# Kernel tuning notes

Measured on AMD Instinct MI355X. Metric: run time of the kernel, lower is better.

The kernel has to match this reference:

```python
import jax, jax.numpy as jnp
import numpy as np

N, DN, DE, L, FE = 1024, 128, 128, 4, 5

def setup_inputs() -> dict:
    key = jax.random.key(0)
    ks = jax.random.split(key, 20)
    f = lambda k, shape, fan: jax.random.normal(k, shape, dtype=jnp.float32) / np.sqrt(fan)
    h = jax.random.normal(ks[0], (1, N, DN), dtype=jnp.float32)
    e = jax.random.normal(ks[1], (1, N, N, DE), dtype=jnp.float32)
    adj = (jax.random.uniform(ks[2], (1, N, N)) < 0.03).astype(jnp.float32)  # sparse-ish dense adjacency
    edge = jax.random.normal(ks[3], (FE,), dtype=jnp.float32)
    return {
        'h': h, 'e': e, 'adj': adj, 'edge': edge,
        # message linear over concat(h_j, e_ij), split into node/edge parts
        'w_msg_h': f(ks[4], (DN, DN), DN + DE),
        'w_msg_e': f(ks[5], (DN, DE), DN + DE),
        'b_msg':   jnp.zeros((DN,), jnp.float32),
        # GRUCell params (torch layout: gates r,z,n stacked)
        'w_ih': f(ks[6], (3 * DN, DN), DN),
        'w_hh': f(ks[7], (3 * DN, DN), DN),
        'b_ih': jnp.zeros((3 * DN,), jnp.float32),
        'b_hh': jnp.zeros((3 * DN,), jnp.float32),
        # gated-sum readout to graph vector of size DE
        'w_gate': f(ks[8], (DE, 2 * DN), 2 * DN),
        'b_gate': jnp.zeros((DE,), jnp.float32),
        'w_out':  f(ks[9], (DE, 2 * DN), 2 * DN),
        'b_out':  jnp.zeros((DE,), jnp.float32),
        # edge embedding (no bias) and final fc
        'w_embed': f(ks[10], (DE, FE), FE),
        'w_fc':    f(ks[11], (DE, 2 * DE), 2 * DE),
        'b_fc':    jnp.zeros((DE,), jnp.float32),
    }


def reference(h, e, adj, edge, w_msg_h, w_msg_e, b_msg, w_ih, w_hh, b_ih, b_hh,
              w_gate, b_gate, w_out, b_out, w_embed, w_fc, b_fc):
    h0 = h
    # edge part of the message is layer-independent: precompute once [1,N,N,DN]
    e_msg = jnp.einsum('bijf,df->bijd', e, w_msg_e)
    for _ in range(L):
        # m_i = sum_j adj_ij * (W_h h_j + W_e e_ij) + b
        m = (jnp.einsum('bij,bjd->bid', adj, h @ w_msg_h.T)
             + jnp.einsum('bij,bijd->bid', adj, e_msg) + b_msg)
        gi = m @ w_ih.T + b_ih
        gh = h @ w_hh.T + b_hh
        gir, giz, gin = jnp.split(gi, 3, axis=-1)
        ghr, ghz, ghn = jnp.split(gh, 3, axis=-1)
        r = jax.nn.sigmoid(gir + ghr)
        z = jax.nn.sigmoid(giz + ghz)
        n = jnp.tanh(gin + r * ghn)
        h = (1.0 - z) * n + z * h
    # gated-sum readout over nodes -> graph vector [1, DE]
    hc = jnp.concatenate([h, h0], axis=-1)
    gv = jnp.sum(jax.nn.sigmoid(hc @ w_gate.T + b_gate) * jnp.tanh(hc @ w_out.T + b_out), axis=1)
    gv = gv.squeeze(0)                      # [DE]
    ee = w_embed @ edge                     # [DE]
    init_edge = jnp.concatenate([gv, ee], axis=-1) @ w_fc.T + b_fc  # [DE]
    return init_edge
```

## Files before the change

kernel.cpp:

```cpp
#include <hip/hip_runtime.h>

__device__ __forceinline__ float sigm(float x){ return 1.f / (1.f + __expf(-x)); }

constexpr int N = 1024, D = 128, CAP = 192;

constexpr int OFF_WT_ME   = 0;
constexpr int OFF_WT_MH   = OFF_WT_ME   + 128*128;
constexpr int OFF_WT_IH   = OFF_WT_MH   + 128*128;
constexpr int OFF_WT_HH   = OFF_WT_IH   + 128*384;
constexpr int OFF_WT_GATE = OFF_WT_HH   + 128*384;
constexpr int OFF_WT_OUT  = OFF_WT_GATE + 256*128;
constexpr int OFF_WT_FC   = OFF_WT_OUT  + 256*128;
constexpr int OFF_EE      = OFF_WT_FC   + 256*128;
constexpr int OFF_GV      = OFF_EE + 128;
constexpr int OFF_EC      = OFF_GV + 128;
constexpr int OFF_HCUR    = OFF_EC   + N*D;
constexpr int OFF_HW      = OFF_HCUR + N*D;
constexpr int OFF_CNT     = OFF_HW   + N*D;
constexpr int OFF_NZI     = OFF_CNT  + N;
constexpr int OFF_NZV     = OFF_NZI  + N*CAP;

constexpr int PT0 = OFF_WT_MH, PT1 = OFF_WT_IH, PT2 = OFF_WT_HH, PT3 = OFF_WT_GATE,
              PT4 = OFF_WT_OUT, PT5 = OFF_WT_FC, PT6 = OFF_EE, PT7 = OFF_GV,
              PT8 = OFF_EC;

__global__ __launch_bounds__(256)
void k_prep(const float* w_me, const float* w_mh, const float* w_ih, const float* w_hh,
            const float* w_gate, const float* w_out, const float* w_fc,
            const float* w_embed, const float* edge, float* ws){
  int idx = blockIdx.x * 256 + threadIdx.x;
  if (idx < PT0)      { int k = idx;       int f = k >> 7, d = k & 127; ws[idx] = w_me[d*128 + f]; }
  else if (idx < PT1) { int k = idx - PT0; int f = k >> 7, d = k & 127; ws[idx] = w_mh[d*128 + f]; }
  else if (idx < PT2) { int k = idx - PT1; int f = k / 384, o = k % 384; ws[idx] = w_ih[o*128 + f]; }
  else if (idx < PT3) { int k = idx - PT2; int f = k / 384, o = k % 384; ws[idx] = w_hh[o*128 + f]; }
  else if (idx < PT4) { int k = idx - PT3; int f = k >> 7, c = k & 127; ws[idx] = w_gate[c*256 + f]; }
  else if (idx < PT5) { int k = idx - PT4; int f = k >> 7, c = k & 127; ws[idx] = w_out[c*256 + f]; }
  else if (idx < PT6) { int k = idx - PT5; int c = k >> 7, o = k & 127; ws[idx] = w_fc[o*256 + c]; }
  else if (idx < PT7) { int c = idx - PT6; float a = 0.f;
                        for (int q = 0; q < 5; ++q) a += w_embed[c*5 + q] * edge[q];
                        ws[idx] = a; }
  else if (idx < PT8) { ws[idx] = 0.f; }
}

__global__ __launch_bounds__(256)
void k_gather(const float* adj, const float* e, const float* h, const float* b_msg, float* ws){
  __shared__ int   cnt_sh;
  __shared__ int   idx_sh[CAP];
  __shared__ float val_sh[CAP];
  __shared__ float red_sh[512];
  __shared__ float ea_sh[128];
  const int i = blockIdx.x, t = threadIdx.x;
  if (t == 0) cnt_sh = 0;
  __syncthreads();
  const float* arow = adj + (size_t)i * N;
  #pragma unroll
  for (int q = 0; q < 4; ++q){
    int j = t + q*256;
    float v = arow[j];
    if (v != 0.f){
      int p = atomicAdd(&cnt_sh, 1);
      if (p < CAP){ idx_sh[p] = j; val_sh[p] = v; }
    }
  }
  __syncthreads();
  const int cnt = min(cnt_sh, CAP);
  int*   cntp = (int*)(ws + OFF_CNT);
  int*   nzi  = (int*)(ws + OFF_NZI);
  float* nzv  = ws + OFF_NZV;
  if (t == 0) cntp[i] = cnt;
  for (int k = t; k < cnt; k += 256){ nzi[(size_t)i*CAP + k] = idx_sh[k]; nzv[(size_t)i*CAP + k] = val_sh[k]; }

  const int lane = t & 63, wv = t >> 6;
  float ax = 0.f, ay = 0.f;
  const float* eb = e + ((size_t)i << 17);
  for (int k = wv; k < cnt; k += 4){
    int j = idx_sh[k]; float v = val_sh[k];
    float2 uu = *(const float2*)(eb + (size_t)j*128 + 2*lane);
    ax += v * uu.x;
    ay += v * uu.y;
  }
  red_sh[wv*128 + 2*lane]     = ax;
  red_sh[wv*128 + 2*lane + 1] = ay;
  __syncthreads();
  if (t < 128) ea_sh[t] = red_sh[t] + red_sh[128+t] + red_sh[256+t] + red_sh[384+t];
  __syncthreads();

  const float* wT = ws + OFF_WT_ME;
  const int d = t & 127, half = t >> 7;
  float acc = 0.f;
  for (int f = half*64; f < half*64 + 64; ++f) acc += ea_sh[f] * wT[f*128 + d];
  red_sh[half*128 + d] = acc;
  __syncthreads();
  if (t < 128){
    ws[OFF_EC   + (size_t)i*128 + t] = red_sh[t] + red_sh[128 + t] + b_msg[t];
    ws[OFF_HCUR + (size_t)i*128 + t] = h[(size_t)i*128 + t];
  }
}

__global__ __launch_bounds__(128)
void k_hw(float* ws){
  __shared__ float h_sh[8][128];
  const int t = threadIdx.x, i0 = blockIdx.x * 8;
  const float* hc = ws + OFF_HCUR;
  #pragma unroll
  for (int n = 0; n < 8; ++n) h_sh[n][t] = hc[(size_t)(i0+n)*128 + t];
  __syncthreads();
  const float* wT = ws + OFF_WT_MH;
  float acc[8] = {};
  for (int f = 0; f < 128; ++f){
    float w = wT[f*128 + t];
    #pragma unroll
    for (int n = 0; n < 8; ++n) acc[n] += w * h_sh[n][f];
  }
  float* hw = ws + OFF_HW;
  #pragma unroll
  for (int n = 0; n < 8; ++n) hw[(size_t)(i0+n)*128 + t] = acc[n];
}

__global__ __launch_bounds__(384)
void k_gru(const float* b_ih, const float* b_hh, float* ws){
  __shared__ float m_sh[4][128], h_sh[4][128];
  __shared__ float sr_sh[4][128], sz_sh[4][128], gn_sh[4][128], hn_sh[4][128];
  const int t = threadIdx.x, i0 = blockIdx.x * 4;
  float* hc = ws + OFF_HCUR;
  const float* hw = ws + OFF_HW;
  const float* ec = ws + OFF_EC;
  const int*   cntp = (const int*)(ws + OFF_CNT);
  const int*   nzi  = (const int*)(ws + OFF_NZI);
  const float* nzv  = ws + OFF_NZV;
  for (int idx = t; idx < 512; idx += 384){
    int n = idx >> 7, c = idx & 127, i = i0 + n;
    h_sh[n][c] = hc[(size_t)i*128 + c];
    float a = ec[(size_t)i*128 + c];
    const int cn = cntp[i];
    const int*   ji = nzi + (size_t)i*CAP;
    const float* jv = nzv + (size_t)i*CAP;
    for (int k = 0; k < cn; ++k) a += jv[k] * hw[(size_t)ji[k]*128 + c];
    m_sh[n][c] = a;
  }
  __syncthreads();
  const float* wi_ = ws + OFF_WT_IH;
  const float* wh_ = ws + OFF_WT_HH;
  float ag[4] = {}, ah[4] = {};
  for (int f = 0; f < 128; ++f){
    float wi = wi_[f*384 + t], wh = wh_[f*384 + t];
    #pragma unroll
    for (int n = 0; n < 4; ++n){ ag[n] += wi * m_sh[n][f]; ah[n] += wh * h_sh[n][f]; }
  }
  const float bi = b_ih[t], bh = b_hh[t];
  if (t < 128){
    #pragma unroll
    for (int n = 0; n < 4; ++n) sr_sh[n][t] = ag[n] + ah[n] + bi + bh;
  } else if (t < 256){
    const int c = t - 128;
    #pragma unroll
    for (int n = 0; n < 4; ++n) sz_sh[n][c] = ag[n] + ah[n] + bi + bh;
  } else {
    const int c = t - 256;
    #pragma unroll
    for (int n = 0; n < 4; ++n){ gn_sh[n][c] = ag[n] + bi; hn_sh[n][c] = ah[n] + bh; }
  }
  __syncthreads();
  for (int idx = t; idx < 512; idx += 384){
    int n = idx >> 7, c = idx & 127;
    float r  = sigm(sr_sh[n][c]);
    float z  = sigm(sz_sh[n][c]);
    float nn = tanhf(gn_sh[n][c] + r * hn_sh[n][c]);
    hc[(size_t)(i0+n)*128 + c] = (1.f - z) * nn + z * h_sh[n][c];
  }
}

__global__ __launch_bounds__(128)
void k_readout(const float* h0, const float* b_gate, const float* b_out, float* ws){
  __shared__ float hc_sh[8][256];
  const int t = threadIdx.x, i0 = blockIdx.x * 8;
  const float* hcur = ws + OFF_HCUR;
  #pragma unroll
  for (int n = 0; n < 8; ++n){
    hc_sh[n][t]       = hcur[(size_t)(i0+n)*128 + t];
    hc_sh[n][128 + t] = h0[(size_t)(i0+n)*128 + t];
  }
  __syncthreads();
  const float* wg_ = ws + OFF_WT_GATE;
  const float* wo_ = ws + OFF_WT_OUT;
  float ag[8] = {}, ao[8] = {};
  for (int f = 0; f < 256; ++f){
    float wg = wg_[f*128 + t], wo = wo_[f*128 + t];
    #pragma unroll
    for (int n = 0; n < 8; ++n){ ag[n] += wg * hc_sh[n][f]; ao[n] += wo * hc_sh[n][f]; }
  }
  const float bg = b_gate[t], bo = b_out[t];
  float s = 0.f;
  #pragma unroll
  for (int n = 0; n < 8; ++n) s += sigm(ag[n] + bg) * tanhf(ao[n] + bo);
  atomicAdd(ws + OFF_GV + t, s);
}

__global__ __launch_bounds__(128)
void k_fc(const float* b_fc, float* out, const float* ws){
  const int o = threadIdx.x;
  const float* wT = ws + OFF_WT_FC;
  const float* gv = ws + OFF_GV;
  const float* ee = ws + OFF_EE;
  float acc = b_fc[o];
  for (int c = 0; c < 128; ++c) acc += gv[c] * wT[c*128 + o];
  for (int c = 0; c < 128; ++c) acc += ee[c] * wT[(128 + c)*128 + o];
  out[o] = acc;
}

extern "C" void kernel_launch(void* const* d_in, const int* in_sizes, int n_in,
                              void* d_out, int out_size, void* d_ws, size_t ws_size,
                              hipStream_t stream){
  const float* h      = (const float*)d_in[0];
  const float* e      = (const float*)d_in[1];
  const float* adj    = (const float*)d_in[2];
  const float* edge   = (const float*)d_in[3];
  const float* w_mh   = (const float*)d_in[4];
  const float* w_me   = (const float*)d_in[5];
  const float* b_msg  = (const float*)d_in[6];
  const float* w_ih   = (const float*)d_in[7];
  const float* w_hh   = (const float*)d_in[8];
  const float* b_ih   = (const float*)d_in[9];
  const float* b_hh   = (const float*)d_in[10];
  const float* w_gate = (const float*)d_in[11];
  const float* b_gate = (const float*)d_in[12];
  const float* w_out  = (const float*)d_in[13];
  const float* b_out  = (const float*)d_in[14];
  const float* w_emb  = (const float*)d_in[15];
  const float* w_fc   = (const float*)d_in[16];
  const float* b_fc   = (const float*)d_in[17];
  float* ws = (float*)d_ws;

  k_prep<<<(PT8 + 255) / 256, 256, 0, stream>>>(w_me, w_mh, w_ih, w_hh, w_gate,
                                                w_out, w_fc, w_emb, edge, ws);
  k_gather<<<N, 256, 0, stream>>>(adj, e, h, b_msg, ws);
  for (int l = 0; l < 4; ++l){
    k_hw <<<N/8, 128, 0, stream>>>(ws);
    k_gru<<<N/4, 384, 0, stream>>>(b_ih, b_hh, ws);
  }
  k_readout<<<N/8, 128, 0, stream>>>(h, b_gate, b_out, ws);
  k_fc<<<1, 128, 0, stream>>>(b_fc, (float*)d_out, ws);
}
```

Before: 804.1 us.

## Fold message weight into GRU input weight and hoist constant edge term

New measurement: 789.0 us. Within noise of the previous version (-1.9%).

```diff
diff --git a/kernel.cpp b/kernel.cpp
--- a/kernel.cpp
+++ b/kernel.cpp
@@ -1,45 +1,56 @@
 #include <hip/hip_runtime.h>
 
+
 __device__ __forceinline__ float sigm(float x){ return 1.f / (1.f + __expf(-x)); }
 
 constexpr int N = 1024, D = 128, CAP = 192;
 
 constexpr int OFF_WT_ME   = 0;
-constexpr int OFF_WT_MH   = OFF_WT_ME   + 128*128;
-constexpr int OFF_WT_IH   = OFF_WT_MH   + 128*128;
+constexpr int OFF_WT_IH   = OFF_WT_ME   + 128*128;
 constexpr int OFF_WT_HH   = OFF_WT_IH   + 128*384;
 constexpr int OFF_WT_GATE = OFF_WT_HH   + 128*384;
 constexpr int OFF_WT_OUT  = OFF_WT_GATE + 256*128;
 constexpr int OFF_WT_FC   = OFF_WT_OUT  + 256*128;
 constexpr int OFF_EE      = OFF_WT_FC   + 256*128;
 constexpr int OFF_GV      = OFF_EE + 128;
-constexpr int OFF_EC      = OFF_GV + 128;
-constexpr int OFF_HCUR    = OFF_EC   + N*D;
-constexpr int OFF_HW      = OFF_HCUR + N*D;
-constexpr int OFF_CNT     = OFF_HW   + N*D;
-constexpr int OFF_NZI     = OFF_CNT  + N;
-constexpr int OFF_NZV     = OFF_NZI  + N*CAP;
-
-constexpr int PT0 = OFF_WT_MH, PT1 = OFF_WT_IH, PT2 = OFF_WT_HH, PT3 = OFF_WT_GATE,
-              PT4 = OFF_WT_OUT, PT5 = OFF_WT_FC, PT6 = OFF_EE, PT7 = OFF_GV,
-              PT8 = OFF_EC;
+constexpr int OFF_WCT     = OFF_GV + 128;
+constexpr int OFF_C       = OFF_WCT + 128*384;
+constexpr int OFF_EC      = OFF_C   + N*384;
+constexpr int OFF_HA      = OFF_EC  + N*D;
+constexpr int OFF_HB      = OFF_HA  + N*D;
+constexpr int OFF_CNT     = OFF_HB  + N*D;
+constexpr int OFF_NZI     = OFF_CNT + N;
+constexpr int OFF_NZV     = OFF_NZI + N*CAP;
+
+constexpr int PT0 = OFF_WT_IH, PT1 = OFF_WT_HH, PT2 = OFF_WT_GATE, PT3 = OFF_WT_OUT,
+              PT4 = OFF_WT_FC, PT5 = OFF_EE, PT6 = OFF_GV, PT7 = OFF_WCT;
 
 __global__ __launch_bounds__(256)
-void k_prep(const float* w_me, const float* w_mh, const float* w_ih, const float* w_hh,
+void k_prep(const float* w_me, const float* w_ih, const float* w_hh,
             const float* w_gate, const float* w_out, const float* w_fc,
             const float* w_embed, const float* edge, float* ws){
   int idx = blockIdx.x * 256 + threadIdx.x;
   if (idx < PT0)      { int k = idx;       int f = k >> 7, d = k & 127; ws[idx] = w_me[d*128 + f]; }
-  else if (idx < PT1) { int k = idx - PT0; int f = k >> 7, d = k & 127; ws[idx] = w_mh[d*128 + f]; }
-  else if (idx < PT2) { int k = idx - PT1; int f = k / 384, o = k % 384; ws[idx] = w_ih[o*128 + f]; }
-  else if (idx < PT3) { int k = idx - PT2; int f = k / 384, o = k % 384; ws[idx] = w_hh[o*128 + f]; }
-  else if (idx < PT4) { int k = idx - PT3; int f = k >> 7, c = k & 127; ws[idx] = w_gate[c*256 + f]; }
-  else if (idx < PT5) { int k = idx - PT4; int f = k >> 7, c = k & 127; ws[idx] = w_out[c*256 + f]; }
-  else if (idx < PT6) { int k = idx - PT5; int c = k >> 7, o = k & 127; ws[idx] = w_fc[o*256 + c]; }
-  else if (idx < PT7) { int c = idx - PT6; float a = 0.f;
+  else if (idx < PT1) { int k = idx - PT0; int f = k / 384, o = k % 384; ws[idx] = w_ih[o*128 + f]; }
+  else if (idx < PT2) { int k = idx - PT1; int f = k / 384, o = k % 384; ws[idx] = w_hh[o*128 + f]; }
+  else if (idx < PT3) { int k = idx - PT2; int f = k >> 7, c = k & 127; ws[idx] = w_gate[c*256 + f]; }
+  else if (idx < PT4) { int k = idx - PT3; int f = k >> 7, c = k & 127; ws[idx] = w_out[c*256 + f]; }
+  else if (idx < PT5) { int k = idx - PT4; int c = k >> 7, o = k & 127; ws[idx] = w_fc[o*256 + c]; }
+  else if (idx < PT6) { int c = idx - PT5; float a = 0.f;
                         for (int q = 0; q < 5; ++q) a += w_embed[c*5 + q] * edge[q];
                         ws[idx] = a; }
-  else if (idx < PT8) { ws[idx] = 0.f; }
+  else if (idx < PT7) { ws[idx] = 0.f; }
+}
+
+__global__ __launch_bounds__(128)
+void k_wc(const float* w_ih, const float* w_mh, float* ws){
+  __shared__ float ih_sh[128];
+  const int o = blockIdx.x, t = threadIdx.x;
+  ih_sh[t] = w_ih[o*128 + t];
+  __syncthreads();
+  float acc = 0.f;
+  for (int d = 0; d < 128; ++d) acc += ih_sh[d] * w_mh[d*128 + t];
+  ws[OFF_WCT + t*384 + o] = acc;
 }
 
 __global__ __launch_bounds__(256)
@@ -92,73 +103,77 @@
   red_sh[half*128 + d] = acc;
   __syncthreads();
   if (t < 128){
-    ws[OFF_EC   + (size_t)i*128 + t] = red_sh[t] + red_sh[128 + t] + b_msg[t];
-    ws[OFF_HCUR + (size_t)i*128 + t] = h[(size_t)i*128 + t];
-  }
-}
-
-__global__ __launch_bounds__(128)
-void k_hw(float* ws){
-  __shared__ float h_sh[8][128];
-  const int t = threadIdx.x, i0 = blockIdx.x * 8;
-  const float* hc = ws + OFF_HCUR;
-  #pragma unroll
-  for (int n = 0; n < 8; ++n) h_sh[n][t] = hc[(size_t)(i0+n)*128 + t];
-  __syncthreads();
-  const float* wT = ws + OFF_WT_MH;
-  float acc[8] = {};
+    ws[OFF_EC + (size_t)i*128 + t] = red_sh[t] + red_sh[128 + t] + b_msg[t];
+    ws[OFF_HA + (size_t)i*128 + t] = h[(size_t)i*128 + t];
+  }
+}
+
+__global__ __launch_bounds__(384)
+void k_cprep(const float* b_ih, float* ws){
+  __shared__ float ec_sh[4][128];
+  const int t = threadIdx.x, i0 = blockIdx.x * 4;
+  const float* ec = ws + OFF_EC;
+  for (int idx = t; idx < 512; idx += 384){
+    int n = idx >> 7, c = idx & 127;
+    ec_sh[n][c] = ec[(size_t)(i0+n)*128 + c];
+  }
+  __syncthreads();
+  const float* wi_ = ws + OFF_WT_IH;
+  float acc[4] = {};
   for (int f = 0; f < 128; ++f){
-    float w = wT[f*128 + t];
-    #pragma unroll
-    for (int n = 0; n < 8; ++n) acc[n] += w * h_sh[n][f];
-  }
-  float* hw = ws + OFF_HW;
-  #pragma unroll
-  for (int n = 0; n < 8; ++n) hw[(size_t)(i0+n)*128 + t] = acc[n];
+    float w = wi_[f*384 + t];
+    #pragma unroll
+    for (int n = 0; n < 4; ++n) acc[n] += w * ec_sh[n][f];
+  }
+  const float bi = b_ih[t];
+  float* C = ws + OFF_C;
+  #pragma unroll
+  for (int n = 0; n < 4; ++n) C[(size_t)(i0+n)*384 + t] = acc[n] + bi;
 }
 
 __global__ __launch_bounds__(384)
-void k_gru(const float* b_ih, const float* b_hh, float* ws){
-  __shared__ float m_sh[4][128], h_sh[4][128];
+void k_layer(const float* b_hh, const float* hA, float* hB, float* ws){
+  __shared__ float hs_sh[4][128], h_sh[4][128];
   __shared__ float sr_sh[4][128], sz_sh[4][128], gn_sh[4][128], hn_sh[4][128];
   const int t = threadIdx.x, i0 = blockIdx.x * 4;
-  float* hc = ws + OFF_HCUR;
-  const float* hw = ws + OFF_HW;
-  const float* ec = ws + OFF_EC;
   const int*   cntp = (const int*)(ws + OFF_CNT);
   const int*   nzi  = (const int*)(ws + OFF_NZI);
   const float* nzv  = ws + OFF_NZV;
   for (int idx = t; idx < 512; idx += 384){
     int n = idx >> 7, c = idx & 127, i = i0 + n;
-    h_sh[n][c] = hc[(size_t)i*128 + c];
-    float a = ec[(size_t)i*128 + c];
+    h_sh[n][c] = hA[(size_t)i*128 + c];
+    float a = 0.f;
     const int cn = cntp[i];
     const int*   ji = nzi + (size_t)i*CAP;
     const float* jv = nzv + (size_t)i*CAP;
-    for (int k = 0; k < cn; ++k) a += jv[k] * hw[(size_t)ji[k]*128 + c];
-    m_sh[n][c] = a;
-  }
-  __syncthreads();
-  const float* wi_ = ws + OFF_WT_IH;
+    for (int k = 0; k < cn; ++k) a += jv[k] * hA[(size_t)ji[k]*128 + c];
+    hs_sh[n][c] = a;
+  }
+  __syncthreads();
+  const float* wc_ = ws + OFF_WCT;
   const float* wh_ = ws + OFF_WT_HH;
   float ag[4] = {}, ah[4] = {};
   for (int f = 0; f < 128; ++f){
-    float wi = wi_[f*384 + t], wh = wh_[f*384 + t];
-    #pragma unroll
-    for (int n = 0; n < 4; ++n){ ag[n] += wi * m_sh[n][f]; ah[n] += wh * h_sh[n][f]; }
-  }
-  const float bi = b_ih[t], bh = b_hh[t];
+    float wi = wc_[f*384 + t], wh = wh_[f*384 + t];
+    #pragma unroll
+    for (int n = 0; n < 4; ++n){ ag[n] += wi * hs_sh[n][f]; ah[n] += wh * h_sh[n][f]; }
+  }
+  const float* C = ws + OFF_C;
+  float cv[4];
+  #pragma unroll
+  for (int n = 0; n < 4; ++n) cv[n] = C[(size_t)(i0+n)*384 + t];
+  const float bh = b_hh[t];
   if (t < 128){
     #pragma unroll
-    for (int n = 0; n < 4; ++n) sr_sh[n][t] = ag[n] + ah[n] + bi + bh;
+    for (int n = 0; n < 4; ++n) sr_sh[n][t] = ag[n] + cv[n] + ah[n] + bh;
   } else if (t < 256){
     const int c = t - 128;
     #pragma unroll
-    for (int n = 0; n < 4; ++n) sz_sh[n][c] = ag[n] + ah[n] + bi + bh;
+    for (int n = 0; n < 4; ++n) sz_sh[n][c] = ag[n] + cv[n] + ah[n] + bh;
   } else {
     const int c = t - 256;
     #pragma unroll
-    for (int n = 0; n < 4; ++n){ gn_sh[n][c] = ag[n] + bi; hn_sh[n][c] = ah[n] + bh; }
+    for (int n = 0; n < 4; ++n){ gn_sh[n][c] = ag[n] + cv[n]; hn_sh[n][c] = ah[n] + bh; }
   }
   __syncthreads();
   for (int idx = t; idx < 512; idx += 384){
@@ -166,7 +181,7 @@
     float r  = sigm(sr_sh[n][c]);
     float z  = sigm(sz_sh[n][c]);
     float nn = tanhf(gn_sh[n][c] + r * hn_sh[n][c]);
-    hc[(size_t)(i0+n)*128 + c] = (1.f - z) * nn + z * h_sh[n][c];
+    hB[(size_t)(i0+n)*128 + c] = (1.f - z) * nn + z * h_sh[n][c];
   }
 }
 
@@ -174,7 +189,7 @@
 void k_readout(const float* h0, const float* b_gate, const float* b_out, float* ws){
   __shared__ float hc_sh[8][256];
   const int t = threadIdx.x, i0 = blockIdx.x * 8;
-  const float* hcur = ws + OFF_HCUR;
+  const float* hcur = ws + OFF_HA;
   #pragma unroll
   for (int n = 0; n < 8; ++n){
     hc_sh[n][t]       = hcur[(size_t)(i0+n)*128 + t];
@@ -231,12 +246,17 @@
   const float* b_fc   = (const float*)d_in[17];
   float* ws = (float*)d_ws;
 
-  k_prep<<<(PT8 + 255) / 256, 256, 0, stream>>>(w_me, w_mh, w_ih, w_hh, w_gate,
-                                                w_out, w_fc, w_emb, edge, ws);
+  k_prep<<<(PT7 + 255) / 256, 256, 0, stream>>>(w_me, w_ih, w_hh, w_gate, w_out,
+                                                w_fc, w_emb, edge, ws);
+  k_wc<<<384, 128, 0, stream>>>(w_ih, w_mh, ws);
   k_gather<<<N, 256, 0, stream>>>(adj, e, h, b_msg, ws);
+  k_cprep<<<N/4, 384, 0, stream>>>(b_ih, ws);
+  float* hA = ws + OFF_HA;
+  float* hB = ws + OFF_HB;
   for (int l = 0; l < 4; ++l){
-    k_hw <<<N/8, 128, 0, stream>>>(ws);
-    k_gru<<<N/4, 384, 0, stream>>>(b_ih, b_hh, ws);
+    const float* src = (l & 1) ? hB : hA;
+    float*       dst = (l & 1) ? hA : hB;
+    k_layer<<<N/4, 384, 0, stream>>>(b_hh, src, dst, ws);
   }
   k_readout<<<N/8, 128, 0, stream>>>(h, b_gate, b_out, ws);
   k_fc<<<1, 128, 0, stream>>>(b_fc, (float*)d_out, ws);
```
